# Optimization experiments

Measured on AMD Instinct MI355X. Metric: run time of the kernel, lower is better.

## Reference

```python
import jax, jax.numpy as jnp
import numpy as np

BOS = 1  # TOKENS['BOS'] assumed


def gru_scan(x_seq, h0, W_ih, W_hh, b_ih, b_hh):
    """PyTorch-style single-layer GRU over time. x_seq: (T,B,H), h0: (B,H)."""
    def step(h, x):
        gi = x @ W_ih.T + b_ih          # (B,3H)
        gh = h @ W_hh.T + b_hh          # (B,3H)
        i_r, i_z, i_n = jnp.split(gi, 3, axis=-1)
        h_r, h_z, h_n = jnp.split(gh, 3, axis=-1)
        r = jax.nn.sigmoid(i_r + h_r)
        z = jax.nn.sigmoid(i_z + h_z)
        n = jnp.tanh(i_n + r * h_n)
        h_new = (1.0 - z) * n + z * h
        return h_new, h_new
    hT, outs = jax.lax.scan(step, h0, x_seq)
    return outs, hT


def setup_inputs() -> dict:
    key = jax.random.key(0)
    ks = jax.random.split(key, 24)
    H = 256
    V = 50003       # user_size + 3
    TAGV = 966
    T_in, T_tgt, T_tag, B = 50, 40, 20, 32
    s = 0.02
    inp = {
        'input_tensor': jax.random.randint(ks[0], (T_in, B), 0, V),
        'target_tensor': jax.random.randint(ks[1], (T_tgt, B), 0, V),
        'tag_tensor': jax.random.randint(ks[2], (T_tag, B), 0, TAGV),
        'enc_emb': jax.random.normal(ks[3], (V, H), jnp.float32) * s,
        'enc_Wih': jax.random.normal(ks[4], (3 * H, H), jnp.float32) * s,
        'enc_Whh': jax.random.normal(ks[5], (3 * H, H), jnp.float32) * s,
        'enc_bih': jax.random.normal(ks[6], (3 * H,), jnp.float32) * s,
        'enc_bhh': jax.random.normal(ks[7], (3 * H,), jnp.float32) * s,
        'tag_emb': jax.random.normal(ks[8], (TAGV, H), jnp.float32) * s,
        'tag_Wih': jax.random.normal(ks[9], (3 * H, H), jnp.float32) * s,
        'tag_Whh': jax.random.normal(ks[10], (3 * H, H), jnp.float32) * s,
        'tag_bih': jax.random.normal(ks[11], (3 * H,), jnp.float32) * s,
        'tag_bhh': jax.random.normal(ks[12], (3 * H,), jnp.float32) * s,
        'proj_W': jax.random.normal(ks[13], (H, 2 * H), jnp.float32) * s,
        'proj_b': jax.random.normal(ks[14], (H,), jnp.float32) * s,
        'dec_Wih': jax.random.normal(ks[15], (3 * H, H), jnp.float32) * s,
        'dec_Whh': jax.random.normal(ks[16], (3 * H, H), jnp.float32) * s,
        'dec_bih': jax.random.normal(ks[17], (3 * H,), jnp.float32) * s,
        'dec_bhh': jax.random.normal(ks[18], (3 * H,), jnp.float32) * s,
        'out_W': jax.random.normal(ks[19], (V, H), jnp.float32) * s,
        'out_b': jax.random.normal(ks[20], (V,), jnp.float32) * s,
    }
    return inp


def reference(input_tensor, target_tensor, tag_tensor,
              enc_emb, enc_Wih, enc_Whh, enc_bih, enc_bhh,
              tag_emb, tag_Wih, tag_Whh, tag_bih, tag_bhh,
              proj_W, proj_b,
              dec_Wih, dec_Whh, dec_bih, dec_bhh,
              out_W, out_b):
    T_in, B = input_tensor.shape
    T_tgt = target_tensor.shape[0]
    H = enc_emb.shape[1]
    h0 = jnp.zeros((B, H), enc_emb.dtype)

    # encoder over input tokens
    _, enc_h = gru_scan(enc_emb[input_tensor], h0, enc_Wih, enc_Whh, enc_bih, enc_bhh)
    # tag encoder
    _, tag_h = gru_scan(tag_emb[tag_tensor], h0, tag_Wih, tag_Whh, tag_bih, tag_bhh)

    # proj(cat(tag_hidden, encoder_hidden)); dropout = identity (eval)
    merged = jnp.concatenate([tag_h, enc_h], axis=-1) @ proj_W.T + proj_b  # (B,H)

    # teacher forcing: decoder inputs = [BOS, target[:-1]]
    dec_in = jnp.concatenate(
        [jnp.full((1, B), BOS, dtype=target_tensor.dtype), target_tensor[:-1]], axis=0)
    dec_x = jax.nn.relu(enc_emb[dec_in])                 # (T_tgt,B,H), shared embedding
    dec_outs, _ = gru_scan(dec_x, merged, dec_Wih, dec_Whh, dec_bih, dec_bhh)
    logits = dec_outs @ out_W.T + out_b                  # (T_tgt,B,V)

    # criterion = CrossEntropyLoss(mean over batch), summed over timesteps
    logp = jax.nn.log_softmax(logits, axis=-1)
    nll = -jnp.take_along_axis(logp, target_tensor[..., None], axis=-1)[..., 0]  # (T_tgt,B)
    decoder_loss = nll.mean(axis=1).sum()
    avg_loss = decoder_loss / T_tgt
    decoder_outputs = logits[:, None, :, :]              # (T_tgt,1,B,V) like torch.stack of unsqueezed
    return (decoder_loss, avg_loss, decoder_outputs)
```

## Files before the change

### kernel.cpp

```cpp
#include <hip/hip_runtime.h>
#include <hip/hip_bf16.h>
#include <math.h>


#define H 256
#define H3 768
#define NBATCH 32
#define TIN 50
#define TTGT 40
#define TTAG 20
#define VSZ 50003
#define VP 50048
#define NT 782
#define MT 1280
#define NGI 330
#define NCVT 12512

typedef float f32x4 __attribute__((ext_vector_type(4)));
typedef short short8 __attribute__((ext_vector_type(8)));

__device__ __forceinline__ float dot4(float4 a, float4 b) {
    return a.x * b.x + a.y * b.y + a.z * b.z + a.w * b.w;
}

__device__ __forceinline__ void bar_lgkm() {
    asm volatile("s_waitcnt lgkmcnt(0)" ::: "memory");
    __builtin_amdgcn_s_barrier();
    __builtin_amdgcn_sched_barrier(0);
}

__global__ void k_prep(const float* eWih, const float* tWih, const float* dWih,
                       const float* projW, const float* eWhh, const float* tWhh,
                       const float* dWhh, float* d0, float* d1, float* d2,
                       float* d3, __hip_bfloat16* p0, __hip_bfloat16* p1,
                       __hip_bfloat16* p2) {
    int which = blockIdx.y;
    if (which < 4) {
        const float* s;
        float* d;
        int N, K;
        switch (which) {
            case 0: s = eWih; d = d0; N = H3; K = H; break;
            case 1: s = tWih; d = d1; N = H3; K = H; break;
            case 2: s = dWih; d = d2; N = H3; K = H; break;
            default: s = projW; d = d3; N = H; K = 2 * H; break;
        }
        int n = blockIdx.x;
        if (n >= N) return;
        for (int k = threadIdx.x; k < K; k += 256)
            d[(size_t)(k >> 2) * (N * 4) + n * 4 + (k & 3)] = s[(size_t)n * K + k];
    } else {
        if (blockIdx.x >= 96) return;
        const float* s = which == 4 ? eWhh : (which == 5 ? tWhh : dWhh);
        __hip_bfloat16* d = which == 4 ? p0 : (which == 5 ? p1 : p2);
        int idx = blockIdx.x * 256 + threadIdx.x;
        int lane = idx & 63;
        int f = (idx >> 6) % 48;
        int w = idx / (48 * 64);
        int ks = f / 6, rem = f % 6;
        int hf = rem / 3, q = rem % 3;
        int row = (q << 8) + (w << 5) + (hf << 4) + (lane & 15);
        int k = (ks << 5) + ((lane >> 4) << 3);
#pragma unroll
        for (int j = 0; j < 8; ++j)
            d[(size_t)idx * 8 + j] = __float2bfloat16(s[(size_t)row * H + k + j]);
    }
}

__global__ __launch_bounds__(256) void k_gi_cvt(
    const int* in_toks, const int* tag_toks, const int* tgt_toks,
    const float* enc_emb, const float* tag_emb, const float* W4e,
    const float* W4t, const float* W4d, const float* bih_e, const float* bhh_e,
    const float* bih_t, const float* bhh_t, const float* bih_d,
    const float* bhh_d, float* gi_e, float* gi_t, float* gi_d,
    const float* outW, __hip_bfloat16* outWb) {
    int bx = blockIdx.x, tid = threadIdx.x;
    if (bx >= NGI) {
        int i4 = ((bx - NGI) * 256 + tid) * 4;
        if (i4 >= VP * H) return;
        int row = i4 >> 8;
        float4 v;
        if (row < VSZ) v = *(const float4*)(outW + i4);
        else v = make_float4(0.f, 0.f, 0.f, 0.f);
        outWb[i4 + 0] = __float2bfloat16(v.x);
        outWb[i4 + 1] = __float2bfloat16(v.y);
        outWb[i4 + 2] = __float2bfloat16(v.z);
        outWb[i4 + 3] = __float2bfloat16(v.w);
        return;
    }
    __shared__ float x[NBATCH][H];
    int g = bx % 3, tt = bx / 3;
    const int* toks;
    const float* emb;
    const float* W4;
    const float* bihp;
    const float* bhhp;
    float* gip;
    int t, mode;
    if (tt < TIN) {
        toks = in_toks; emb = enc_emb; W4 = W4e; bihp = bih_e; bhhp = bhh_e;
        gip = gi_e; t = tt; mode = 0;
    } else if (tt < TIN + TTAG) {
        toks = tag_toks; emb = tag_emb; W4 = W4t; bihp = bih_t; bhhp = bhh_t;
        gip = gi_t; t = tt - TIN; mode = 0;
    } else {
        toks = tgt_toks; emb = enc_emb; W4 = W4d; bihp = bih_d; bhhp = bhh_d;
        gip = gi_d; t = tt - TIN - TTAG; mode = 2;
    }
    for (int b = 0; b < NBATCH; ++b) {
        int tok;
        if (mode == 2) tok = (t == 0) ? 1 : toks[(t - 1) * NBATCH + b];
        else tok = toks[t * NBATCH + b];
        float v = emb[(size_t)tok * H + tid];
        if (mode == 2) v = fmaxf(v, 0.0f);
        x[b][tid] = v;
    }
    __syncthreads();
    int nb_ = tid & 63, mg = tid >> 6;
    float acc[4][8];
#pragma unroll
    for (int j = 0; j < 4; ++j)
#pragma unroll
        for (int mi = 0; mi < 8; ++mi) acc[j][mi] = 0.f;
    for (int k4 = 0; k4 < 64; ++k4) {
        const float4* wrow = (const float4*)(W4 + (size_t)k4 * 3072);
        float4 w0 = wrow[g * 256 + nb_];
        float4 w1 = wrow[g * 256 + nb_ + 64];
        float4 w2 = wrow[g * 256 + nb_ + 128];
        float4 w3 = wrow[g * 256 + nb_ + 192];
#pragma unroll
        for (int mi = 0; mi < 8; ++mi) {
            float4 xv = *(const float4*)&x[mg * 8 + mi][k4 * 4];
            acc[0][mi] += dot4(xv, w0);
            acc[1][mi] += dot4(xv, w1);
            acc[2][mi] += dot4(xv, w2);
            acc[3][mi] += dot4(xv, w3);
        }
    }
#pragma unroll
    for (int j = 0; j < 4; ++j) {
        int n = g * 256 + nb_ + j * 64;
        float bv = bihp[n] + (g < 2 ? bhhp[n] : 0.0f);
        int nn = n & 255;
        int ww = nn >> 5, hf = (nn >> 4) & 1, lrr = nn & 15;
#pragma unroll
        for (int mi = 0; mi < 8; ++mi) {
            int bm = mg * 8 + mi;
            int locb = bm >> 4, lmm = bm & 15;
            int lgg = lmm >> 2, reg = lmm & 3;
            size_t idx = ((size_t)(t * 2 + locb) * 8 + ww) * 2048 +
                         hf * 1024 + reg * 256 + (lgg * 16 + lrr) * 4 + g;
            gip[idx] = acc[j][mi] + bv;
        }
    }
}

__global__ __launch_bounds__(512) void k_scan(
    int nset1,
    const float* gi1, const __hip_bfloat16* W1, const float* bhh1,
    const float* h01, float* hT1, __hip_bfloat16* out1, int T1,
    const float* gi2, const __hip_bfloat16* W2, const float* bhh2,
    const float* h02, float* hT2, __hip_bfloat16* out2, int T2) {
    __shared__ uint4 WL[8 * 12 * 64];
    __shared__ uint4 HBF[2][512];

    int blk = blockIdx.x, tid = threadIdx.x;
    const float *gip, *bhh, *h0;
    const __hip_bfloat16* Wg;
    float* hTp;
    __hip_bfloat16* outp;
    int T, loc;
    if (blk < nset1) {
        gip = gi1; Wg = W1; bhh = bhh1; h0 = h01; hTp = hT1; outp = out1;
        T = T1; loc = blk;
    } else {
        gip = gi2; Wg = W2; bhh = bhh2; h0 = h02; hTp = hT2; outp = out2;
        T = T2; loc = blk - nset1;
    }
    int mb = loc * 16;
    int w = tid >> 6, lane = tid & 63, lr = lane & 15, lg = lane >> 4;

    short8 wreg[36];
    const uint4* Wg4 = (const uint4*)Wg;
#pragma unroll
    for (int f = 0; f < 36; ++f) {
        uint4 v = Wg4[(size_t)(w * 48 + f) * 64 + lane];
        wreg[f] = *(short8*)&v;
    }
#pragma unroll
    for (int i = 0; i < 12; ++i)
        WL[(w * 12 + i) * 64 + lane] = Wg4[(size_t)(w * 48 + 36 + i) * 64 + lane];

    float bnv[2];
    bnv[0] = bhh[512 + w * 32 + lr];
    bnv[1] = bhh[512 + w * 32 + 16 + lr];

    float hprev[8];
    short* HB16 = (short*)HBF;
#pragma unroll
    for (int hf = 0; hf < 2; ++hf)
#pragma unroll
        for (int reg = 0; reg < 4; ++reg) {
            int row = lg * 4 + reg, col = w * 32 + hf * 16 + lr;
            float hv = h0 ? h0[(size_t)(mb + row) * H + col] : 0.0f;
            hprev[hf * 4 + reg] = hv;
            __hip_bfloat16 q = __float2bfloat16(hv);
            int slot = (w * 4 + hf * 2 + (lr >> 3)) ^ (row & 7);
            HB16[row * 256 + slot * 8 + (lr & 7)] = *(short*)&q;
        }
    float4 gv[8];
    {
        const float* gp = gip + ((size_t)loc * 8 + w) * 2048;
#pragma unroll
        for (int i = 0; i < 8; ++i)
            gv[i] = *(const float4*)(gp + (i >> 2) * 1024 + (i & 3) * 256 + lane * 4);
    }
    __syncthreads();

    const short8* HSbase = (const short8*)HBF;
    const short8* WLs = (const short8*)WL;
    for (int t = 0; t < T; ++t) {
        int p = t & 1, p2 = p ^ 1;
        const short8* HS = HSbase + p * 512;
        f32x4 acc[6];
        acc[0] = (f32x4){0.f, 0.f, 0.f, 0.f};
        acc[1] = acc[0];
        acc[2] = (f32x4){bnv[0], bnv[0], bnv[0], bnv[0]};
        acc[3] = acc[0];
        acc[4] = acc[0];
        acc[5] = (f32x4){bnv[1], bnv[1], bnv[1], bnv[1]};
#pragma unroll
        for (int ks = 0; ks < 6; ++ks) {
            short8 a = HS[lr * 32 + ((ks * 4 + lg) ^ (lr & 7))];
#pragma unroll
            for (int hf = 0; hf < 2; ++hf)
#pragma unroll
                for (int q = 0; q < 3; ++q)
                    acc[hf * 3 + q] = __builtin_amdgcn_mfma_f32_16x16x32_bf16(
                        a, wreg[ks * 6 + hf * 3 + q], acc[hf * 3 + q], 0, 0, 0);
        }
#pragma unroll
        for (int ks = 6; ks < 8; ++ks) {
            short8 a = HS[lr * 32 + ((ks * 4 + lg) ^ (lr & 7))];
#pragma unroll
            for (int hf = 0; hf < 2; ++hf)
#pragma unroll
                for (int q = 0; q < 3; ++q) {
                    short8 bv = WLs[(w * 12 + (ks - 6) * 6 + hf * 3 + q) * 64 + lane];
                    acc[hf * 3 + q] = __builtin_amdgcn_mfma_f32_16x16x32_bf16(
                        a, bv, acc[hf * 3 + q], 0, 0, 0);
                }
        }
#pragma unroll
        for (int hf = 0; hf < 2; ++hf)
#pragma unroll
            for (int reg = 0; reg < 4; ++reg) {
                float4 g4 = gv[hf * 4 + reg];
                float er = __expf(-(g4.x + acc[hf * 3 + 0][reg]));
                float r = __builtin_amdgcn_rcpf(1.0f + er);
                float ez = __expf(-(g4.y + acc[hf * 3 + 1][reg]));
                float z = __builtin_amdgcn_rcpf(1.0f + ez);
                float xx = g4.z + r * acc[hf * 3 + 2][reg];
                float e2 = __expf(-2.0f * fabsf(xx));
                float nv = copysignf((1.0f - e2) * __builtin_amdgcn_rcpf(1.0f + e2), xx);
                float hnew = (1.0f - z) * nv + z * hprev[hf * 4 + reg];
                hprev[hf * 4 + reg] = hnew;
                __hip_bfloat16 qb = __float2bfloat16(hnew);
                int row = lg * 4 + reg;
                int slot = (w * 4 + hf * 2 + (lr >> 3)) ^ (row & 7);
                HB16[p2 * 4096 + row * 256 + slot * 8 + (lr & 7)] = *(short*)&qb;
            }
        if (t + 1 < T) {
            const float* gp = gip + ((size_t)((t + 1) * 2 + loc) * 8 + w) * 2048;
#pragma unroll
            for (int i = 0; i < 8; ++i)
                gv[i] = *(const float4*)(gp + (i >> 2) * 1024 + (i & 3) * 256 + lane * 4);
        }
        if (outp && t >= 1) {
            int lb = tid >> 5, ch = tid & 31;
            short8 hv = HSbase[p * 512 + lb * 32 + (ch ^ (lb & 7))];
            *(short8*)(outp + (size_t)((t - 1) * NBATCH + mb + lb) * H + ch * 8) = hv;
        }
        bar_lgkm();
    }
    if (outp) {
        int lb = tid >> 5, ch = tid & 31;
        short8 hv = HSbase[(T & 1) * 512 + lb * 32 + (ch ^ (lb & 7))];
        *(short8*)(outp + (size_t)((T - 1) * NBATCH + mb + lb) * H + ch * 8) = hv;
    }
    if (hTp) {
#pragma unroll
        for (int hf = 0; hf < 2; ++hf)
#pragma unroll
            for (int reg = 0; reg < 4; ++reg) {
                int row = lg * 4 + reg, col = w * 32 + hf * 16 + lr;
                hTp[(size_t)(mb + row) * H + col] = hprev[hf * 4 + reg];
            }
    }
}

__global__ void k_proj(const float* tag_h, const float* enc_h,
                       const float* W4p, const float* pb, float* merged) {
    __shared__ float c[2 * H];
    int b = blockIdx.x, tid = threadIdx.x;
    c[tid] = tag_h[b * H + tid];
    c[H + tid] = enc_h[b * H + tid];
    __syncthreads();
    float acc = 0.f;
#pragma unroll 4
    for (int k4 = 0; k4 < 128; ++k4) {
        float4 cv = *(const float4*)&c[k4 * 4];
        float4 wv = ((const float4*)(W4p + (size_t)k4 * 1024))[tid];
        acc += dot4(cv, wv);
    }
    merged[b * H + tid] = acc + pb[tid];
}

__global__ __launch_bounds__(256) void k_logits(const __hip_bfloat16* A,
                                                const __hip_bfloat16* Bw,
                                                const float* bias, float* dout,
                                                float* pmax, float* psum) {
    __shared__ uint4 bsm[2048];
    __shared__ float cst[4][16][68];
    int bid = blockIdx.x;
    int wg = (bid & 7) * 1955 + (bid >> 3);
    int nblk = wg / 20, mblk = wg % 20;
    int m0 = mblk * 64, n0 = nblk * 64;
    int tid = threadIdx.x;
    int wave = tid >> 6, lane = tid & 63, lr = lane & 15, lg = lane >> 4;
    const uint4* Bg = (const uint4*)(Bw + (size_t)n0 * H);
#pragma unroll
    for (int i = 0; i < 8; ++i) {
        int c = tid + i * 256;
        int r = c >> 5, g = c & 31;
        bsm[(r << 5) | (g ^ (r & 7))] = Bg[c];
    }
    short8 areg[8];
    const uint4* Ar = (const uint4*)(A + (size_t)(m0 + wave * 16 + lr) * H);
#pragma unroll
    for (int ks = 0; ks < 8; ++ks) {
        uint4 v = Ar[ks * 4 + lg];
        areg[ks] = *(short8*)&v;
    }
    float biasv[4];
    bool valid[4];
#pragma unroll
    for (int ns = 0; ns < 4; ++ns) {
        int n = n0 + ns * 16 + lr;
        valid[ns] = (n < VSZ);
        biasv[ns] = valid[ns] ? bias[n] : 0.f;
    }
    __syncthreads();
    f32x4 acc[4];
#pragma unroll
    for (int ns = 0; ns < 4; ++ns) acc[ns] = (f32x4){0.f, 0.f, 0.f, 0.f};
    const short8* L = (const short8*)bsm;
#pragma unroll
    for (int ks = 0; ks < 8; ++ks) {
        int ga = ks * 4 + lg;
#pragma unroll
        for (int ns = 0; ns < 4; ++ns) {
            int rb = ns * 16 + lr;
            acc[ns] = __builtin_amdgcn_mfma_f32_16x16x32_bf16(
                areg[ks], L[(rb << 5) | (ga ^ (rb & 7))], acc[ns], 0, 0, 0);
        }
    }
    float* cw = &cst[wave][0][0];
#pragma unroll
    for (int reg = 0; reg < 4; ++reg) {
        int m = m0 + wave * 16 + lg * 4 + reg;
        float v[4];
        float rm = -INFINITY;
#pragma unroll
        for (int ns = 0; ns < 4; ++ns) {
            v[ns] = acc[ns][reg] + biasv[ns];
            if (valid[ns]) rm = fmaxf(rm, v[ns]);
            cw[(lg * 4 + reg) * 68 + ns * 16 + lr] = v[ns];
        }
        for (int off = 1; off < 16; off <<= 1) rm = fmaxf(rm, __shfl_xor(rm, off));
        float se = 0.f;
#pragma unroll
        for (int ns = 0; ns < 4; ++ns)
            if (valid[ns]) se += __expf(v[ns] - rm);
        for (int off = 1; off < 16; off <<= 1) se += __shfl_xor(se, off);
        if (lr == 0) {
            pmax[(size_t)m * NT + nblk] = rm;
            psum[(size_t)m * NT + nblk] = se;
        }
    }
    float* dbase = dout + 2 + (size_t)(m0 + wave * 16) * VSZ + n0;
    bool colok = (n0 + lane < VSZ);
#pragma unroll
    for (int rl = 0; rl < 16; ++rl) {
        float val = cst[wave][rl][lane];
        if (colok) dbase[(size_t)rl * VSZ + lane] = val;
    }
}

__global__ void k_lse(const float* pmax, const float* psum, float* lse) {
    int m = blockIdx.x, tid = threadIdx.x;
    __shared__ float sm[4];
    float lm = -INFINITY;
    for (int i = tid; i < NT; i += 256) lm = fmaxf(lm, pmax[(size_t)m * NT + i]);
    for (int off = 1; off < 64; off <<= 1) lm = fmaxf(lm, __shfl_xor(lm, off));
    if ((tid & 63) == 0) sm[tid >> 6] = lm;
    __syncthreads();
    float M = fmaxf(fmaxf(sm[0], sm[1]), fmaxf(sm[2], sm[3]));
    __syncthreads();
    float s = 0.f;
    for (int i = tid; i < NT; i += 256)
        s += psum[(size_t)m * NT + i] * __expf(pmax[(size_t)m * NT + i] - M);
    for (int off = 1; off < 64; off <<= 1) s += __shfl_xor(s, off);
    if ((tid & 63) == 0) sm[tid >> 6] = s;
    __syncthreads();
    if (tid == 0) lse[m] = M + logf(sm[0] + sm[1] + sm[2] + sm[3]);
}

__global__ void k_loss(const float* lse, const int* tgt, float* dout) {
    int tid = threadIdx.x;
    __shared__ float sm[4];
    float s = 0.f;
    for (int m = tid; m < MT; m += 256) {
        int tg = tgt[m];
        s += lse[m] - dout[2 + (size_t)m * VSZ + tg];
    }
    for (int off = 1; off < 64; off <<= 1) s += __shfl_xor(s, off);
    if ((tid & 63) == 0) sm[tid >> 6] = s;
    __syncthreads();
    if (tid == 0) {
        float total = sm[0] + sm[1] + sm[2] + sm[3];
        dout[0] = total / 32.0f;
        dout[1] = total / 1280.0f;
    }
}

extern "C" void kernel_launch(void* const* d_in, const int* in_sizes, int n_in,
                              void* d_out, int out_size, void* d_ws,
                              size_t ws_size, hipStream_t stream) {
    const int* input_tensor = (const int*)d_in[0];
    const int* target_tensor = (const int*)d_in[1];
    const int* tag_tensor = (const int*)d_in[2];
    const float* enc_emb = (const float*)d_in[3];
    const float* enc_Wih = (const float*)d_in[4];
    const float* enc_Whh = (const float*)d_in[5];
    const float* enc_bih = (const float*)d_in[6];
    const float* enc_bhh = (const float*)d_in[7];
    const float* tag_emb = (const float*)d_in[8];
    const float* tag_Wih = (const float*)d_in[9];
    const float* tag_Whh = (const float*)d_in[10];
    const float* tag_bih = (const float*)d_in[11];
    const float* tag_bhh = (const float*)d_in[12];
    const float* proj_W = (const float*)d_in[13];
    const float* proj_b = (const float*)d_in[14];
    const float* dec_Wih = (const float*)d_in[15];
    const float* dec_Whh = (const float*)d_in[16];
    const float* dec_bih = (const float*)d_in[17];
    const float* dec_bhh = (const float*)d_in[18];
    const float* out_W = (const float*)d_in[19];
    const float* out_b = (const float*)d_in[20];

    char* wsb = (char*)d_ws;
    size_t o = 0;
    auto alloc = [&](size_t bytes) {
        size_t r = o;
        o += (bytes + 511) & ~(size_t)511;
        return r;
    };
    float* W4_enc_ih = (float*)(wsb + alloc(H3 * H * 4));
    float* W4_tag_ih = (float*)(wsb + alloc(H3 * H * 4));
    float* W4_dec_ih = (float*)(wsb + alloc(H3 * H * 4));
    float* W4_proj   = (float*)(wsb + alloc(H * 2 * H * 4));
    float* gi_enc = (float*)(wsb + alloc((size_t)TIN * 131072));
    float* gi_tag = (float*)(wsb + alloc((size_t)TTAG * 131072));
    float* gi_dec = (float*)(wsb + alloc((size_t)TTGT * 131072));
    float* enc_h  = (float*)(wsb + alloc(NBATCH * H * 4));
    float* tag_h  = (float*)(wsb + alloc(NBATCH * H * 4));
    float* merged = (float*)(wsb + alloc(NBATCH * H * 4));
    float* lse    = (float*)(wsb + alloc(MT * 4));
    __hip_bfloat16* Wp_enc = (__hip_bfloat16*)(wsb + alloc(H3 * H * 2));
    __hip_bfloat16* Wp_tag = (__hip_bfloat16*)(wsb + alloc(H3 * H * 2));
    __hip_bfloat16* Wp_dec = (__hip_bfloat16*)(wsb + alloc(H3 * H * 2));
    __hip_bfloat16* outWb  = (__hip_bfloat16*)(wsb + alloc((size_t)VP * H * 2));
    __hip_bfloat16* decA   = (__hip_bfloat16*)(wsb + alloc((size_t)MT * H * 2));
    float* pmax = (float*)(wsb + alloc((size_t)MT * NT * 4));
    float* psum = (float*)(wsb + alloc((size_t)MT * NT * 4));

    float* dout = (float*)d_out;

    k_prep<<<dim3(H3, 7), 256, 0, stream>>>(
        enc_Wih, tag_Wih, dec_Wih, proj_W, enc_Whh, tag_Whh, dec_Whh,
        W4_enc_ih, W4_tag_ih, W4_dec_ih, W4_proj, Wp_enc, Wp_tag, Wp_dec);

    k_gi_cvt<<<NGI + NCVT, 256, 0, stream>>>(
        input_tensor, tag_tensor, target_tensor, enc_emb, tag_emb, W4_enc_ih,
        W4_tag_ih, W4_dec_ih, enc_bih, enc_bhh, tag_bih, tag_bhh, dec_bih,
        dec_bhh, gi_enc, gi_tag, gi_dec, out_W, outWb);

    k_scan<<<4, 512, 0, stream>>>(
        2, gi_enc, Wp_enc, enc_bhh, nullptr, enc_h, nullptr, TIN,
        gi_tag, Wp_tag, tag_bhh, nullptr, tag_h, nullptr, TTAG);

    k_proj<<<NBATCH, 256, 0, stream>>>(tag_h, enc_h, W4_proj, proj_b, merged);

    k_scan<<<2, 512, 0, stream>>>(
        2, gi_dec, Wp_dec, dec_bhh, merged, nullptr, decA, TTGT,
        nullptr, nullptr, nullptr, nullptr, nullptr, nullptr, 0);

    k_logits<<<NT * 20, 256, 0, stream>>>(decA, outWb, out_b, dout, pmax, psum);

    k_lse<<<MT, 256, 0, stream>>>(pmax, psum, lse);

    k_loss<<<1, 256, 0, stream>>>(lse, target_tensor, dout);
}
```

Measured before the change: 506.5 us.

## Fuse decoder scan with logits GEMM via progress flags and bf16 gate inputs

Merges the decoder GRU scan and the vocabulary logits GEMM into one kernel. Two scan blocks publish per-timestep progress through atomic flags, and the GEMM blocks spin-wait on those flags, so the logit tiles for early timesteps can start while later timesteps are still being computed. The precomputed input-gate activations are stored in bf16 instead of fp32 to cut scan-side memory traffic. More recurrent weight fragments are kept in registers rather than LDS, and the logits tiles are widened to 512 threads covering two M blocks. This risks deadlock if the scan blocks are not scheduled ahead of the spinning GEMM blocks, and adds bf16 rounding to the gate inputs.

```diff
diff --git a/kernel.cpp b/kernel.cpp
--- a/kernel.cpp
+++ b/kernel.cpp
@@ -23,6 +23,11 @@
     return a.x * b.x + a.y * b.y + a.z * b.z + a.w * b.w;
 }
 
+__device__ __forceinline__ float bf2f(short s) {
+    unsigned int u = ((unsigned int)(unsigned short)s) << 16;
+    return __builtin_bit_cast(float, u);
+}
+
 __device__ __forceinline__ void bar_lgkm() {
     asm volatile("s_waitcnt lgkmcnt(0)" ::: "memory");
     __builtin_amdgcn_s_barrier();
@@ -33,8 +38,10 @@
                        const float* projW, const float* eWhh, const float* tWhh,
                        const float* dWhh, float* d0, float* d1, float* d2,
                        float* d3, __hip_bfloat16* p0, __hip_bfloat16* p1,
-                       __hip_bfloat16* p2) {
+                       __hip_bfloat16* p2, int* prog) {
     int which = blockIdx.y;
+    if (which == 0 && blockIdx.x == 0 && threadIdx.x < 2)
+        prog[threadIdx.x] = 0;
     if (which < 4) {
         const float* s;
         float* d;
@@ -72,8 +79,8 @@
     const float* enc_emb, const float* tag_emb, const float* W4e,
     const float* W4t, const float* W4d, const float* bih_e, const float* bhh_e,
     const float* bih_t, const float* bhh_t, const float* bih_d,
-    const float* bhh_d, float* gi_e, float* gi_t, float* gi_d,
-    const float* outW, __hip_bfloat16* outWb) {
+    const float* bhh_d, __hip_bfloat16* gi_e, __hip_bfloat16* gi_t,
+    __hip_bfloat16* gi_d, const float* outW, __hip_bfloat16* outWb) {
     int bx = blockIdx.x, tid = threadIdx.x;
     if (bx >= NGI) {
         int i4 = ((bx - NGI) * 256 + tid) * 4;
@@ -95,7 +102,7 @@
     const float* W4;
     const float* bihp;
     const float* bhhp;
-    float* gip;
+    __hip_bfloat16* gip;
     int t, mode;
     if (tt < TIN) {
         toks = in_toks; emb = enc_emb; W4 = W4e; bihp = bih_e; bhhp = bhh_e;
@@ -150,46 +157,43 @@
             int lgg = lmm >> 2, reg = lmm & 3;
             size_t idx = ((size_t)(t * 2 + locb) * 8 + ww) * 2048 +
                          hf * 1024 + reg * 256 + (lgg * 16 + lrr) * 4 + g;
-            gip[idx] = acc[j][mi] + bv;
+            gip[idx] = __float2bfloat16(acc[j][mi] + bv);
         }
     }
 }
 
 __global__ __launch_bounds__(512) void k_scan(
     int nset1,
-    const float* gi1, const __hip_bfloat16* W1, const float* bhh1,
-    const float* h01, float* hT1, __hip_bfloat16* out1, int T1,
-    const float* gi2, const __hip_bfloat16* W2, const float* bhh2,
-    const float* h02, float* hT2, __hip_bfloat16* out2, int T2) {
-    __shared__ uint4 WL[8 * 12 * 64];
+    const __hip_bfloat16* gi1, const __hip_bfloat16* W1, const float* bhh1,
+    float* hT1, int T1,
+    const __hip_bfloat16* gi2, const __hip_bfloat16* W2, const float* bhh2,
+    float* hT2, int T2) {
+    __shared__ uint4 WL[6 * 8 * 64];
     __shared__ uint4 HBF[2][512];
 
     int blk = blockIdx.x, tid = threadIdx.x;
-    const float *gip, *bhh, *h0;
-    const __hip_bfloat16* Wg;
+    const __hip_bfloat16 *gip, *Wg;
+    const float* bhh;
     float* hTp;
-    __hip_bfloat16* outp;
     int T, loc;
     if (blk < nset1) {
-        gip = gi1; Wg = W1; bhh = bhh1; h0 = h01; hTp = hT1; outp = out1;
-        T = T1; loc = blk;
+        gip = gi1; Wg = W1; bhh = bhh1; hTp = hT1; T = T1; loc = blk;
     } else {
-        gip = gi2; Wg = W2; bhh = bhh2; h0 = h02; hTp = hT2; outp = out2;
-        T = T2; loc = blk - nset1;
+        gip = gi2; Wg = W2; bhh = bhh2; hTp = hT2; T = T2; loc = blk - nset1;
     }
     int mb = loc * 16;
     int w = tid >> 6, lane = tid & 63, lr = lane & 15, lg = lane >> 4;
 
-    short8 wreg[36];
+    short8 wreg[42];
     const uint4* Wg4 = (const uint4*)Wg;
 #pragma unroll
-    for (int f = 0; f < 36; ++f) {
+    for (int f = 0; f < 42; ++f) {
         uint4 v = Wg4[(size_t)(w * 48 + f) * 64 + lane];
         wreg[f] = *(short8*)&v;
     }
 #pragma unroll
-    for (int i = 0; i < 12; ++i)
-        WL[(w * 12 + i) * 64 + lane] = Wg4[(size_t)(w * 48 + 36 + i) * 64 + lane];
+    for (int i = 0; i < 6; ++i)
+        WL[(w * 6 + i) * 64 + lane] = Wg4[(size_t)(w * 48 + 42 + i) * 64 + lane];
 
     float bnv[2];
     bnv[0] = bhh[512 + w * 32 + lr];
@@ -201,19 +205,17 @@
     for (int hf = 0; hf < 2; ++hf)
 #pragma unroll
         for (int reg = 0; reg < 4; ++reg) {
-            int row = lg * 4 + reg, col = w * 32 + hf * 16 + lr;
-            float hv = h0 ? h0[(size_t)(mb + row) * H + col] : 0.0f;
-            hprev[hf * 4 + reg] = hv;
-            __hip_bfloat16 q = __float2bfloat16(hv);
+            int row = lg * 4 + reg;
+            hprev[hf * 4 + reg] = 0.0f;
             int slot = (w * 4 + hf * 2 + (lr >> 3)) ^ (row & 7);
-            HB16[row * 256 + slot * 8 + (lr & 7)] = *(short*)&q;
-        }
-    float4 gv[8];
+            HB16[row * 256 + slot * 8 + (lr & 7)] = 0;
+        }
+    uint2 gv[8];
     {
-        const float* gp = gip + ((size_t)loc * 8 + w) * 2048;
+        const __hip_bfloat16* gp = gip + ((size_t)loc * 8 + w) * 2048;
 #pragma unroll
         for (int i = 0; i < 8; ++i)
-            gv[i] = *(const float4*)(gp + (i >> 2) * 1024 + (i & 3) * 256 + lane * 4);
+            gv[i] = *(const uint2*)(gp + (i >> 2) * 1024 + (i & 3) * 256 + lane * 4);
     }
     __syncthreads();
 
@@ -230,7 +232,7 @@
         acc[4] = acc[0];
         acc[5] = (f32x4){bnv[1], bnv[1], bnv[1], bnv[1]};
 #pragma unroll
-        for (int ks = 0; ks < 6; ++ks) {
+        for (int ks = 0; ks < 7; ++ks) {
             short8 a = HS[lr * 32 + ((ks * 4 + lg) ^ (lr & 7))];
 #pragma unroll
             for (int hf = 0; hf < 2; ++hf)
@@ -239,14 +241,13 @@
                     acc[hf * 3 + q] = __builtin_amdgcn_mfma_f32_16x16x32_bf16(
                         a, wreg[ks * 6 + hf * 3 + q], acc[hf * 3 + q], 0, 0, 0);
         }
-#pragma unroll
-        for (int ks = 6; ks < 8; ++ks) {
-            short8 a = HS[lr * 32 + ((ks * 4 + lg) ^ (lr & 7))];
+        {
+            short8 a = HS[lr * 32 + ((28 + lg) ^ (lr & 7))];
 #pragma unroll
             for (int hf = 0; hf < 2; ++hf)
 #pragma unroll
                 for (int q = 0; q < 3; ++q) {
-                    short8 bv = WLs[(w * 12 + (ks - 6) * 6 + hf * 3 + q) * 64 + lane];
+                    short8 bv = WLs[(w * 6 + hf * 3 + q) * 64 + lane];
                     acc[hf * 3 + q] = __builtin_amdgcn_mfma_f32_16x16x32_bf16(
                         a, bv, acc[hf * 3 + q], 0, 0, 0);
                 }
@@ -255,12 +256,15 @@
         for (int hf = 0; hf < 2; ++hf)
 #pragma unroll
             for (int reg = 0; reg < 4; ++reg) {
-                float4 g4 = gv[hf * 4 + reg];
-                float er = __expf(-(g4.x + acc[hf * 3 + 0][reg]));
+                uint2 u = gv[hf * 4 + reg];
+                float gr = bf2f((short)(u.x & 0xffff));
+                float gz = bf2f((short)(u.x >> 16));
+                float gn = bf2f((short)(u.y & 0xffff));
+                float er = __expf(-(gr + acc[hf * 3 + 0][reg]));
                 float r = __builtin_amdgcn_rcpf(1.0f + er);
-                float ez = __expf(-(g4.y + acc[hf * 3 + 1][reg]));
+                float ez = __expf(-(gz + acc[hf * 3 + 1][reg]));
                 float z = __builtin_amdgcn_rcpf(1.0f + ez);
-                float xx = g4.z + r * acc[hf * 3 + 2][reg];
+                float xx = gn + r * acc[hf * 3 + 2][reg];
                 float e2 = __expf(-2.0f * fabsf(xx));
                 float nv = copysignf((1.0f - e2) * __builtin_amdgcn_rcpf(1.0f + e2), xx);
                 float hnew = (1.0f - z) * nv + z * hprev[hf * 4 + reg];
@@ -271,22 +275,13 @@
                 HB16[p2 * 4096 + row * 256 + slot * 8 + (lr & 7)] = *(short*)&qb;
             }
         if (t + 1 < T) {
-            const float* gp = gip + ((size_t)((t + 1) * 2 + loc) * 8 + w) * 2048;
+            const __hip_bfloat16* gp =
+                gip + ((size_t)((t + 1) * 2 + loc) * 8 + w) * 2048;
 #pragma unroll
             for (int i = 0; i < 8; ++i)
-                gv[i] = *(const float4*)(gp + (i >> 2) * 1024 + (i & 3) * 256 + lane * 4);
-        }
-        if (outp && t >= 1) {
-            int lb = tid >> 5, ch = tid & 31;
-            short8 hv = HSbase[p * 512 + lb * 32 + (ch ^ (lb & 7))];
-            *(short8*)(outp + (size_t)((t - 1) * NBATCH + mb + lb) * H + ch * 8) = hv;
+                gv[i] = *(const uint2*)(gp + (i >> 2) * 1024 + (i & 3) * 256 + lane * 4);
         }
         bar_lgkm();
-    }
-    if (outp) {
-        int lb = tid >> 5, ch = tid & 31;
-        short8 hv = HSbase[(T & 1) * 512 + lb * 32 + (ch ^ (lb & 7))];
-        *(short8*)(outp + (size_t)((T - 1) * NBATCH + mb + lb) * H + ch * 8) = hv;
     }
     if (hTp) {
 #pragma unroll
@@ -316,31 +311,165 @@
     merged[b * H + tid] = acc + pb[tid];
 }
 
-__global__ __launch_bounds__(256) void k_logits(const __hip_bfloat16* A,
-                                                const __hip_bfloat16* Bw,
-                                                const float* bias, float* dout,
-                                                float* pmax, float* psum) {
-    __shared__ uint4 bsm[2048];
-    __shared__ float cst[4][16][68];
-    int bid = blockIdx.x;
-    int wg = (bid & 7) * 1955 + (bid >> 3);
-    int nblk = wg / 20, mblk = wg % 20;
-    int m0 = mblk * 64, n0 = nblk * 64;
+__global__ __launch_bounds__(512) void k_declog(
+    const __hip_bfloat16* gi_dec, const __hip_bfloat16* Wdec,
+    const float* dec_bhh, const float* merged, __hip_bfloat16* decA,
+    int* prog, const __hip_bfloat16* Bw, const float* bias, float* dout,
+    float* pmax, float* psum) {
+    __shared__ __align__(16) char smem[67584];
     int tid = threadIdx.x;
     int wave = tid >> 6, lane = tid & 63, lr = lane & 15, lg = lane >> 4;
+
+    if (blockIdx.x < 2) {
+        uint4* WL = (uint4*)smem;
+        uint4* HBF = (uint4*)(smem + 49152);
+        short* HB16 = (short*)HBF;
+        int loc = blockIdx.x, mb = loc * 16, w = wave;
+        const int T = TTGT;
+
+        short8 wreg[42];
+        const uint4* Wg4 = (const uint4*)Wdec;
+#pragma unroll
+        for (int f = 0; f < 42; ++f) {
+            uint4 v = Wg4[(size_t)(w * 48 + f) * 64 + lane];
+            wreg[f] = *(short8*)&v;
+        }
+#pragma unroll
+        for (int i = 0; i < 6; ++i)
+            WL[(w * 6 + i) * 64 + lane] =
+                Wg4[(size_t)(w * 48 + 42 + i) * 64 + lane];
+
+        float bnv[2];
+        bnv[0] = dec_bhh[512 + w * 32 + lr];
+        bnv[1] = dec_bhh[512 + w * 32 + 16 + lr];
+
+        float hprev[8];
+#pragma unroll
+        for (int hf = 0; hf < 2; ++hf)
+#pragma unroll
+            for (int reg = 0; reg < 4; ++reg) {
+                int row = lg * 4 + reg, col = w * 32 + hf * 16 + lr;
+                float hv = merged[(size_t)(mb + row) * H + col];
+                hprev[hf * 4 + reg] = hv;
+                __hip_bfloat16 q = __float2bfloat16(hv);
+                int slot = (w * 4 + hf * 2 + (lr >> 3)) ^ (row & 7);
+                HB16[row * 256 + slot * 8 + (lr & 7)] = *(short*)&q;
+            }
+        uint2 gv[8];
+        {
+            const __hip_bfloat16* gp = gi_dec + ((size_t)loc * 8 + w) * 2048;
+#pragma unroll
+            for (int i = 0; i < 8; ++i)
+                gv[i] = *(const uint2*)(gp + (i >> 2) * 1024 + (i & 3) * 256 + lane * 4);
+        }
+        __syncthreads();
+
+        const short8* HSbase = (const short8*)HBF;
+        const short8* WLs = (const short8*)WL;
+        for (int t = 0; t < T; ++t) {
+            int p = t & 1, p2 = p ^ 1;
+            const short8* HS = HSbase + p * 512;
+            f32x4 acc[6];
+            acc[0] = (f32x4){0.f, 0.f, 0.f, 0.f};
+            acc[1] = acc[0];
+            acc[2] = (f32x4){bnv[0], bnv[0], bnv[0], bnv[0]};
+            acc[3] = acc[0];
+            acc[4] = acc[0];
+            acc[5] = (f32x4){bnv[1], bnv[1], bnv[1], bnv[1]};
+#pragma unroll
+            for (int ks = 0; ks < 7; ++ks) {
+                short8 a = HS[lr * 32 + ((ks * 4 + lg) ^ (lr & 7))];
+#pragma unroll
+                for (int hf = 0; hf < 2; ++hf)
+#pragma unroll
+                    for (int q = 0; q < 3; ++q)
+                        acc[hf * 3 + q] = __builtin_amdgcn_mfma_f32_16x16x32_bf16(
+                            a, wreg[ks * 6 + hf * 3 + q], acc[hf * 3 + q], 0, 0, 0);
+            }
+            {
+                short8 a = HS[lr * 32 + ((28 + lg) ^ (lr & 7))];
+#pragma unroll
+                for (int hf = 0; hf < 2; ++hf)
+#pragma unroll
+                    for (int q = 0; q < 3; ++q) {
+                        short8 bv = WLs[(w * 6 + hf * 3 + q) * 64 + lane];
+                        acc[hf * 3 + q] = __builtin_amdgcn_mfma_f32_16x16x32_bf16(
+                            a, bv, acc[hf * 3 + q], 0, 0, 0);
+                    }
+            }
+#pragma unroll
+            for (int hf = 0; hf < 2; ++hf)
+#pragma unroll
+                for (int reg = 0; reg < 4; ++reg) {
+                    uint2 u = gv[hf * 4 + reg];
+                    float gr = bf2f((short)(u.x & 0xffff));
+                    float gz = bf2f((short)(u.x >> 16));
+                    float gn = bf2f((short)(u.y & 0xffff));
+                    float er = __expf(-(gr + acc[hf * 3 + 0][reg]));
+                    float r = __builtin_amdgcn_rcpf(1.0f + er);
+                    float ez = __expf(-(gz + acc[hf * 3 + 1][reg]));
+                    float z = __builtin_amdgcn_rcpf(1.0f + ez);
+                    float xx = gn + r * acc[hf * 3 + 2][reg];
+                    float e2 = __expf(-2.0f * fabsf(xx));
+                    float nv = copysignf(
+                        (1.0f - e2) * __builtin_amdgcn_rcpf(1.0f + e2), xx);
+                    float hnew = (1.0f - z) * nv + z * hprev[hf * 4 + reg];
+                    hprev[hf * 4 + reg] = hnew;
+                    __hip_bfloat16 qb = __float2bfloat16(hnew);
+                    int row = lg * 4 + reg;
+                    int slot = (w * 4 + hf * 2 + (lr >> 3)) ^ (row & 7);
+                    HB16[p2 * 4096 + row * 256 + slot * 8 + (lr & 7)] = *(short*)&qb;
+                }
+            if (t >= 1) {
+                int lb = tid >> 5, ch = tid & 31;
+                short8 hv = HSbase[p * 512 + lb * 32 + (ch ^ (lb & 7))];
+                *(short8*)(decA + (size_t)((t - 1) * NBATCH + mb + lb) * H + ch * 8) = hv;
+            }
+            bool pub = ((t & 1) == 0) && t >= 2;
+            if (pub) asm volatile("s_waitcnt vmcnt(0)" ::: "memory");
+            if (t + 1 < T) {
+                const __hip_bfloat16* gp =
+                    gi_dec + ((size_t)((t + 1) * 2 + loc) * 8 + w) * 2048;
+#pragma unroll
+                for (int i = 0; i < 8; ++i)
+                    gv[i] = *(const uint2*)(gp + (i >> 2) * 1024 + (i & 3) * 256 + lane * 4);
+            }
+            bar_lgkm();
+            if (pub && tid == 0) {
+                __threadfence();
+                __hip_atomic_store(&prog[loc], t, __ATOMIC_RELEASE,
+                                   __HIP_MEMORY_SCOPE_AGENT);
+            }
+        }
+        {
+            int lb = tid >> 5, ch = tid & 31;
+            short8 hv = HSbase[(T & 1) * 512 + lb * 32 + (ch ^ (lb & 7))];
+            *(short8*)(decA + (size_t)((T - 1) * NBATCH + mb + lb) * H + ch * 8) = hv;
+        }
+        asm volatile("s_waitcnt vmcnt(0)" ::: "memory");
+        __syncthreads();
+        if (tid == 0) {
+            __threadfence();
+            __hip_atomic_store(&prog[loc], TTGT, __ATOMIC_RELEASE,
+                               __HIP_MEMORY_SCOPE_AGENT);
+        }
+        return;
+    }
+
+    uint4* bsm = (uint4*)smem;
+    float* cst = (float*)(smem + 32768);
+    int lbid = blockIdx.x - 2;
+    int mpair = lbid / NT, nblk = lbid % NT;
+    int wg2 = wave >> 2, wsub = wave & 3;
+    int mblk = mpair * 2 + wg2;
+    int m0 = mblk * 64, n0 = nblk * 64;
+
     const uint4* Bg = (const uint4*)(Bw + (size_t)n0 * H);
 #pragma unroll
-    for (int i = 0; i < 8; ++i) {
-        int c = tid + i * 256;
+    for (int i = 0; i < 4; ++i) {
+        int c = tid + i * 512;
         int r = c >> 5, g = c & 31;
         bsm[(r << 5) | (g ^ (r & 7))] = Bg[c];
-    }
-    short8 areg[8];
-    const uint4* Ar = (const uint4*)(A + (size_t)(m0 + wave * 16 + lr) * H);
-#pragma unroll
-    for (int ks = 0; ks < 8; ++ks) {
-        uint4 v = Ar[ks * 4 + lg];
-        areg[ks] = *(short8*)&v;
     }
     float biasv[4];
     bool valid[4];
@@ -350,7 +479,23 @@
         valid[ns] = (n < VSZ);
         biasv[ns] = valid[ns] ? bias[n] : 0.f;
     }
-    __syncthreads();
+    if (tid == 0) {
+        int need = 4 * mpair + 4;
+        while (__hip_atomic_load(&prog[0], __ATOMIC_ACQUIRE,
+                                 __HIP_MEMORY_SCOPE_AGENT) < need ||
+               __hip_atomic_load(&prog[1], __ATOMIC_ACQUIRE,
+                                 __HIP_MEMORY_SCOPE_AGENT) < need)
+            __builtin_amdgcn_s_sleep(8);
+    }
+    __syncthreads();
+
+    short8 areg[8];
+    const uint4* Ar = (const uint4*)(decA + (size_t)(m0 + wsub * 16 + lr) * H);
+#pragma unroll
+    for (int ks = 0; ks < 8; ++ks) {
+        uint4 v = Ar[ks * 4 + lg];
+        areg[ks] = *(short8*)&v;
+    }
     f32x4 acc[4];
 #pragma unroll
     for (int ns = 0; ns < 4; ++ns) acc[ns] = (f32x4){0.f, 0.f, 0.f, 0.f};
@@ -365,10 +510,10 @@
                 areg[ks], L[(rb << 5) | (ga ^ (rb & 7))], acc[ns], 0, 0, 0);
         }
     }
-    float* cw = &cst[wave][0][0];
+    float* cw = cst + wave * (16 * 68);
 #pragma unroll
     for (int reg = 0; reg < 4; ++reg) {
-        int m = m0 + wave * 16 + lg * 4 + reg;
+        int m = m0 + wsub * 16 + lg * 4 + reg;
         float v[4];
         float rm = -INFINITY;
 #pragma unroll
@@ -388,11 +533,11 @@
             psum[(size_t)m * NT + nblk] = se;
         }
     }
-    float* dbase = dout + 2 + (size_t)(m0 + wave * 16) * VSZ + n0;
+    float* dbase = dout + 2 + (size_t)(m0 + wsub * 16) * VSZ + n0;
     bool colok = (n0 + lane < VSZ);
 #pragma unroll
     for (int rl = 0; rl < 16; ++rl) {
-        float val = cst[wave][rl][lane];
+        float val = cw[rl * 68 + lane];
         if (colok) dbase[(size_t)rl * VSZ + lane] = val;
     }
 }
@@ -470,13 +615,14 @@
     float* W4_tag_ih = (float*)(wsb + alloc(H3 * H * 4));
     float* W4_dec_ih = (float*)(wsb + alloc(H3 * H * 4));
     float* W4_proj   = (float*)(wsb + alloc(H * 2 * H * 4));
-    float* gi_enc = (float*)(wsb + alloc((size_t)TIN * 131072));
-    float* gi_tag = (float*)(wsb + alloc((size_t)TTAG * 131072));
-    float* gi_dec = (float*)(wsb + alloc((size_t)TTGT * 131072));
+    __hip_bfloat16* gi_enc = (__hip_bfloat16*)(wsb + alloc((size_t)TIN * 65536));
+    __hip_bfloat16* gi_tag = (__hip_bfloat16*)(wsb + alloc((size_t)TTAG * 65536));
+    __hip_bfloat16* gi_dec = (__hip_bfloat16*)(wsb + alloc((size_t)TTGT * 65536));
     float* enc_h  = (float*)(wsb + alloc(NBATCH * H * 4));
     float* tag_h  = (float*)(wsb + alloc(NBATCH * H * 4));
     float* merged = (float*)(wsb + alloc(NBATCH * H * 4));
     float* lse    = (float*)(wsb + alloc(MT * 4));
+    int*   prog   = (int*)(wsb + alloc(64 * 4));
     __hip_bfloat16* Wp_enc = (__hip_bfloat16*)(wsb + alloc(H3 * H * 2));
     __hip_bfloat16* Wp_tag = (__hip_bfloat16*)(wsb + alloc(H3 * H * 2));
     __hip_bfloat16* Wp_dec = (__hip_bfloat16*)(wsb + alloc(H3 * H * 2));
@@ -489,7 +635,8 @@
 
     k_prep<<<dim3(H3, 7), 256, 0, stream>>>(
         enc_Wih, tag_Wih, dec_Wih, proj_W, enc_Whh, tag_Whh, dec_Whh,
-        W4_enc_ih, W4_tag_ih, W4_dec_ih, W4_proj, Wp_enc, Wp_tag, Wp_dec);
+        W4_enc_ih, W4_tag_ih, W4_dec_ih, W4_proj, Wp_enc, Wp_tag, Wp_dec,
+        prog);
 
     k_gi_cvt<<<NGI + NCVT, 256, 0, stream>>>(
         input_tensor, tag_tensor, target_tensor, enc_emb, tag_emb, W4_enc_ih,
@@ -497,16 +644,14 @@
         dec_bhh, gi_enc, gi_tag, gi_dec, out_W, outWb);
 
     k_scan<<<4, 512, 0, stream>>>(
-        2, gi_enc, Wp_enc, enc_bhh, nullptr, enc_h, nullptr, TIN,
-        gi_tag, Wp_tag, tag_bhh, nullptr, tag_h, nullptr, TTAG);
+        2, gi_enc, Wp_enc, enc_bhh, enc_h, TIN,
+        gi_tag, Wp_tag, tag_bhh, tag_h, TTAG);
 
     k_proj<<<NBATCH, 256, 0, stream>>>(tag_h, enc_h, W4_proj, proj_b, merged);
 
-    k_scan<<<2, 512, 0, stream>>>(
-        2, gi_dec, Wp_dec, dec_bhh, merged, nullptr, decA, TTGT,
-        nullptr, nullptr, nullptr, nullptr, nullptr, nullptr, 0);
-
-    k_logits<<<NT * 20, 256, 0, stream>>>(decA, outWb, out_b, dout, pmax, psum);
+    k_declog<<<2 + 10 * NT, 512, 0, stream>>>(
+        gi_dec, Wp_dec, dec_bhh, merged, decA, prog, outWb, out_b, dout,
+        pmax, psum);
 
     k_lse<<<MT, 256, 0, stream>>>(pmax, psum, lse);
 
```

After: 608.4 us. 20.1% more time.

## Split GRU scan across 16 waves with bf16 gate inputs and streaming logits stores

Applied to the files above, without the earlier changes.

The recurrent scan kernel now uses 1024 threads (16 waves), each owning 16 hidden columns instead of 32. This halves the per-wave MFMA chain and register-held weights on the latency-bound serial recurrence. The precomputed input-gate activations are stored and read as bf16 instead of fp32, halving their traffic, at some cost in precision. Logit stores use nontemporal hints to avoid polluting cache with the large output.

```diff
diff --git a/kernel.cpp b/kernel.cpp
--- a/kernel.cpp
+++ b/kernel.cpp
@@ -21,6 +21,11 @@
 
 __device__ __forceinline__ float dot4(float4 a, float4 b) {
     return a.x * b.x + a.y * b.y + a.z * b.z + a.w * b.w;
+}
+
+__device__ __forceinline__ float bf2f(short s) {
+    unsigned int u = ((unsigned int)(unsigned short)s) << 16;
+    return __builtin_bit_cast(float, u);
 }
 
 __device__ __forceinline__ void bar_lgkm() {
@@ -55,11 +60,10 @@
         __hip_bfloat16* d = which == 4 ? p0 : (which == 5 ? p1 : p2);
         int idx = blockIdx.x * 256 + threadIdx.x;
         int lane = idx & 63;
-        int f = (idx >> 6) % 48;
-        int w = idx / (48 * 64);
-        int ks = f / 6, rem = f % 6;
-        int hf = rem / 3, q = rem % 3;
-        int row = (q << 8) + (w << 5) + (hf << 4) + (lane & 15);
+        int f = (idx >> 6) % 24;
+        int w = idx / (24 * 64);
+        int ks = f / 3, q = f % 3;
+        int row = (q << 8) + (w << 4) + (lane & 15);
         int k = (ks << 5) + ((lane >> 4) << 3);
 #pragma unroll
         for (int j = 0; j < 8; ++j)
@@ -72,8 +76,8 @@
     const float* enc_emb, const float* tag_emb, const float* W4e,
     const float* W4t, const float* W4d, const float* bih_e, const float* bhh_e,
     const float* bih_t, const float* bhh_t, const float* bih_d,
-    const float* bhh_d, float* gi_e, float* gi_t, float* gi_d,
-    const float* outW, __hip_bfloat16* outWb) {
+    const float* bhh_d, __hip_bfloat16* gi_e, __hip_bfloat16* gi_t,
+    __hip_bfloat16* gi_d, const float* outW, __hip_bfloat16* outWb) {
     int bx = blockIdx.x, tid = threadIdx.x;
     if (bx >= NGI) {
         int i4 = ((bx - NGI) * 256 + tid) * 4;
@@ -95,7 +99,7 @@
     const float* W4;
     const float* bihp;
     const float* bhhp;
-    float* gip;
+    __hip_bfloat16* gip;
     int t, mode;
     if (tt < TIN) {
         toks = in_toks; emb = enc_emb; W4 = W4e; bihp = bih_e; bhhp = bhh_e;
@@ -142,31 +146,31 @@
         int n = g * 256 + nb_ + j * 64;
         float bv = bihp[n] + (g < 2 ? bhhp[n] : 0.0f);
         int nn = n & 255;
-        int ww = nn >> 5, hf = (nn >> 4) & 1, lrr = nn & 15;
+        int ww = nn >> 4, lrr = nn & 15;
 #pragma unroll
         for (int mi = 0; mi < 8; ++mi) {
             int bm = mg * 8 + mi;
             int locb = bm >> 4, lmm = bm & 15;
             int lgg = lmm >> 2, reg = lmm & 3;
-            size_t idx = ((size_t)(t * 2 + locb) * 8 + ww) * 2048 +
-                         hf * 1024 + reg * 256 + (lgg * 16 + lrr) * 4 + g;
-            gip[idx] = acc[j][mi] + bv;
-        }
-    }
-}
-
-__global__ __launch_bounds__(512) void k_scan(
+            size_t idx = ((size_t)(t * 2 + locb) * 16 + ww) * 1024 +
+                         reg * 256 + (lgg * 16 + lrr) * 4 + g;
+            gip[idx] = __float2bfloat16(acc[j][mi] + bv);
+        }
+    }
+}
+
+__global__ __launch_bounds__(1024) void k_scan(
     int nset1,
-    const float* gi1, const __hip_bfloat16* W1, const float* bhh1,
+    const __hip_bfloat16* gi1, const __hip_bfloat16* W1, const float* bhh1,
     const float* h01, float* hT1, __hip_bfloat16* out1, int T1,
-    const float* gi2, const __hip_bfloat16* W2, const float* bhh2,
+    const __hip_bfloat16* gi2, const __hip_bfloat16* W2, const float* bhh2,
     const float* h02, float* hT2, __hip_bfloat16* out2, int T2) {
-    __shared__ uint4 WL[8 * 12 * 64];
+    __shared__ uint4 WL[16 * 6 * 64];
     __shared__ uint4 HBF[2][512];
 
     int blk = blockIdx.x, tid = threadIdx.x;
-    const float *gip, *bhh, *h0;
-    const __hip_bfloat16* Wg;
+    const __hip_bfloat16 *gip, *Wg;
+    const float *bhh, *h0;
     float* hTp;
     __hip_bfloat16* outp;
     int T, loc;
@@ -180,40 +184,37 @@
     int mb = loc * 16;
     int w = tid >> 6, lane = tid & 63, lr = lane & 15, lg = lane >> 4;
 
-    short8 wreg[36];
+    short8 wreg[18];
     const uint4* Wg4 = (const uint4*)Wg;
 #pragma unroll
-    for (int f = 0; f < 36; ++f) {
-        uint4 v = Wg4[(size_t)(w * 48 + f) * 64 + lane];
+    for (int f = 0; f < 18; ++f) {
+        uint4 v = Wg4[(size_t)(w * 24 + f) * 64 + lane];
         wreg[f] = *(short8*)&v;
     }
 #pragma unroll
-    for (int i = 0; i < 12; ++i)
-        WL[(w * 12 + i) * 64 + lane] = Wg4[(size_t)(w * 48 + 36 + i) * 64 + lane];
-
-    float bnv[2];
-    bnv[0] = bhh[512 + w * 32 + lr];
-    bnv[1] = bhh[512 + w * 32 + 16 + lr];
-
-    float hprev[8];
+    for (int i = 0; i < 6; ++i)
+        WL[(w * 6 + i) * 64 + lane] = Wg4[(size_t)(w * 24 + 18 + i) * 64 + lane];
+
+    float bnv = bhh[512 + w * 16 + lr];
+
+    float hprev[4];
     short* HB16 = (short*)HBF;
 #pragma unroll
-    for (int hf = 0; hf < 2; ++hf)
-#pragma unroll
-        for (int reg = 0; reg < 4; ++reg) {
-            int row = lg * 4 + reg, col = w * 32 + hf * 16 + lr;
-            float hv = h0 ? h0[(size_t)(mb + row) * H + col] : 0.0f;
-            hprev[hf * 4 + reg] = hv;
-            __hip_bfloat16 q = __float2bfloat16(hv);
-            int slot = (w * 4 + hf * 2 + (lr >> 3)) ^ (row & 7);
-            HB16[row * 256 + slot * 8 + (lr & 7)] = *(short*)&q;
-        }
-    float4 gv[8];
+    for (int reg = 0; reg < 4; ++reg) {
+        int row = lg * 4 + reg, col = w * 16 + lr;
+        float hv = h0 ? h0[(size_t)(mb + row) * H + col] : 0.0f;
+        hprev[reg] = hv;
+        __hip_bfloat16 q = __float2bfloat16(hv);
+        int ch = w * 2 + (lr >> 3);
+        int slot = ch ^ (row & 7);
+        HB16[row * 256 + slot * 8 + (lr & 7)] = *(short*)&q;
+    }
+    uint2 gv[4];
     {
-        const float* gp = gip + ((size_t)loc * 8 + w) * 2048;
-#pragma unroll
-        for (int i = 0; i < 8; ++i)
-            gv[i] = *(const float4*)(gp + (i >> 2) * 1024 + (i & 3) * 256 + lane * 4);
+        const __hip_bfloat16* gp = gip + ((size_t)loc * 16 + w) * 1024;
+#pragma unroll
+        for (int reg = 0; reg < 4; ++reg)
+            gv[reg] = *(const uint2*)(gp + reg * 256 + lane * 4);
     }
     __syncthreads();
 
@@ -222,80 +223,74 @@
     for (int t = 0; t < T; ++t) {
         int p = t & 1, p2 = p ^ 1;
         const short8* HS = HSbase + p * 512;
-        f32x4 acc[6];
+        f32x4 acc[3];
         acc[0] = (f32x4){0.f, 0.f, 0.f, 0.f};
         acc[1] = acc[0];
-        acc[2] = (f32x4){bnv[0], bnv[0], bnv[0], bnv[0]};
-        acc[3] = acc[0];
-        acc[4] = acc[0];
-        acc[5] = (f32x4){bnv[1], bnv[1], bnv[1], bnv[1]};
+        acc[2] = (f32x4){bnv, bnv, bnv, bnv};
 #pragma unroll
         for (int ks = 0; ks < 6; ++ks) {
             short8 a = HS[lr * 32 + ((ks * 4 + lg) ^ (lr & 7))];
 #pragma unroll
-            for (int hf = 0; hf < 2; ++hf)
-#pragma unroll
-                for (int q = 0; q < 3; ++q)
-                    acc[hf * 3 + q] = __builtin_amdgcn_mfma_f32_16x16x32_bf16(
-                        a, wreg[ks * 6 + hf * 3 + q], acc[hf * 3 + q], 0, 0, 0);
+            for (int q = 0; q < 3; ++q)
+                acc[q] = __builtin_amdgcn_mfma_f32_16x16x32_bf16(
+                    a, wreg[ks * 3 + q], acc[q], 0, 0, 0);
         }
 #pragma unroll
         for (int ks = 6; ks < 8; ++ks) {
             short8 a = HS[lr * 32 + ((ks * 4 + lg) ^ (lr & 7))];
 #pragma unroll
-            for (int hf = 0; hf < 2; ++hf)
-#pragma unroll
-                for (int q = 0; q < 3; ++q) {
-                    short8 bv = WLs[(w * 12 + (ks - 6) * 6 + hf * 3 + q) * 64 + lane];
-                    acc[hf * 3 + q] = __builtin_amdgcn_mfma_f32_16x16x32_bf16(
-                        a, bv, acc[hf * 3 + q], 0, 0, 0);
-                }
-        }
-#pragma unroll
-        for (int hf = 0; hf < 2; ++hf)
-#pragma unroll
-            for (int reg = 0; reg < 4; ++reg) {
-                float4 g4 = gv[hf * 4 + reg];
-                float er = __expf(-(g4.x + acc[hf * 3 + 0][reg]));
-                float r = __builtin_amdgcn_rcpf(1.0f + er);
-                float ez = __expf(-(g4.y + acc[hf * 3 + 1][reg]));
-                float z = __builtin_amdgcn_rcpf(1.0f + ez);
-                float xx = g4.z + r * acc[hf * 3 + 2][reg];
-                float e2 = __expf(-2.0f * fabsf(xx));
-                float nv = copysignf((1.0f - e2) * __builtin_amdgcn_rcpf(1.0f + e2), xx);
-                float hnew = (1.0f - z) * nv + z * hprev[hf * 4 + reg];
-                hprev[hf * 4 + reg] = hnew;
-                __hip_bfloat16 qb = __float2bfloat16(hnew);
-                int row = lg * 4 + reg;
-                int slot = (w * 4 + hf * 2 + (lr >> 3)) ^ (row & 7);
-                HB16[p2 * 4096 + row * 256 + slot * 8 + (lr & 7)] = *(short*)&qb;
+            for (int q = 0; q < 3; ++q) {
+                short8 bv = WLs[(w * 6 + (ks - 6) * 3 + q) * 64 + lane];
+                acc[q] = __builtin_amdgcn_mfma_f32_16x16x32_bf16(
+                    a, bv, acc[q], 0, 0, 0);
             }
+        }
+#pragma unroll
+        for (int reg = 0; reg < 4; ++reg) {
+            uint2 u = gv[reg];
+            float gr = bf2f((short)(u.x & 0xffff));
+            float gz = bf2f((short)(u.x >> 16));
+            float gn = bf2f((short)(u.y & 0xffff));
+            float er = __expf(-(gr + acc[0][reg]));
+            float r = __builtin_amdgcn_rcpf(1.0f + er);
+            float ez = __expf(-(gz + acc[1][reg]));
+            float z = __builtin_amdgcn_rcpf(1.0f + ez);
+            float xx = gn + r * acc[2][reg];
+            float e2 = __expf(-2.0f * fabsf(xx));
+            float nv = copysignf((1.0f - e2) * __builtin_amdgcn_rcpf(1.0f + e2), xx);
+            float hnew = (1.0f - z) * nv + z * hprev[reg];
+            hprev[reg] = hnew;
+            __hip_bfloat16 qb = __float2bfloat16(hnew);
+            int row = lg * 4 + reg;
+            int ch = w * 2 + (lr >> 3);
+            int slot = ch ^ (row & 7);
+            HB16[p2 * 4096 + row * 256 + slot * 8 + (lr & 7)] = *(short*)&qb;
+        }
         if (t + 1 < T) {
-            const float* gp = gip + ((size_t)((t + 1) * 2 + loc) * 8 + w) * 2048;
-#pragma unroll
-            for (int i = 0; i < 8; ++i)
-                gv[i] = *(const float4*)(gp + (i >> 2) * 1024 + (i & 3) * 256 + lane * 4);
-        }
-        if (outp && t >= 1) {
-            int lb = tid >> 5, ch = tid & 31;
-            short8 hv = HSbase[p * 512 + lb * 32 + (ch ^ (lb & 7))];
-            *(short8*)(outp + (size_t)((t - 1) * NBATCH + mb + lb) * H + ch * 8) = hv;
+            const __hip_bfloat16* gp =
+                gip + ((size_t)((t + 1) * 2 + loc) * 16 + w) * 1024;
+#pragma unroll
+            for (int reg = 0; reg < 4; ++reg)
+                gv[reg] = *(const uint2*)(gp + reg * 256 + lane * 4);
+        }
+        if (outp && t >= 1 && tid < 512) {
+            int lb = tid >> 5, ch2 = tid & 31;
+            short8 hv = HSbase[p * 512 + lb * 32 + (ch2 ^ (lb & 7))];
+            *(short8*)(outp + (size_t)((t - 1) * NBATCH + mb + lb) * H + ch2 * 8) = hv;
         }
         bar_lgkm();
     }
-    if (outp) {
-        int lb = tid >> 5, ch = tid & 31;
-        short8 hv = HSbase[(T & 1) * 512 + lb * 32 + (ch ^ (lb & 7))];
-        *(short8*)(outp + (size_t)((T - 1) * NBATCH + mb + lb) * H + ch * 8) = hv;
+    if (outp && tid < 512) {
+        int lb = tid >> 5, ch2 = tid & 31;
+        short8 hv = HSbase[(T & 1) * 512 + lb * 32 + (ch2 ^ (lb & 7))];
+        *(short8*)(outp + (size_t)((T - 1) * NBATCH + mb + lb) * H + ch2 * 8) = hv;
     }
     if (hTp) {
 #pragma unroll
-        for (int hf = 0; hf < 2; ++hf)
-#pragma unroll
-            for (int reg = 0; reg < 4; ++reg) {
-                int row = lg * 4 + reg, col = w * 32 + hf * 16 + lr;
-                hTp[(size_t)(mb + row) * H + col] = hprev[hf * 4 + reg];
-            }
+        for (int reg = 0; reg < 4; ++reg) {
+            int row = lg * 4 + reg, col = w * 16 + lr;
+            hTp[(size_t)(mb + row) * H + col] = hprev[reg];
+        }
     }
 }
 
@@ -393,7 +388,8 @@
 #pragma unroll
     for (int rl = 0; rl < 16; ++rl) {
         float val = cst[wave][rl][lane];
-        if (colok) dbase[(size_t)rl * VSZ + lane] = val;
+        if (colok)
+            __builtin_nontemporal_store(val, &dbase[(size_t)rl * VSZ + lane]);
     }
 }
 
@@ -470,9 +466,9 @@
     float* W4_tag_ih = (float*)(wsb + alloc(H3 * H * 4));
     float* W4_dec_ih = (float*)(wsb + alloc(H3 * H * 4));
     float* W4_proj   = (float*)(wsb + alloc(H * 2 * H * 4));
-    float* gi_enc = (float*)(wsb + alloc((size_t)TIN * 131072));
-    float* gi_tag = (float*)(wsb + alloc((size_t)TTAG * 131072));
-    float* gi_dec = (float*)(wsb + alloc((size_t)TTGT * 131072));
+    __hip_bfloat16* gi_enc = (__hip_bfloat16*)(wsb + alloc((size_t)TIN * 65536));
+    __hip_bfloat16* gi_tag = (__hip_bfloat16*)(wsb + alloc((size_t)TTAG * 65536));
+    __hip_bfloat16* gi_dec = (__hip_bfloat16*)(wsb + alloc((size_t)TTGT * 65536));
     float* enc_h  = (float*)(wsb + alloc(NBATCH * H * 4));
     float* tag_h  = (float*)(wsb + alloc(NBATCH * H * 4));
     float* merged = (float*)(wsb + alloc(NBATCH * H * 4));
@@ -496,13 +492,13 @@
         W4_tag_ih, W4_dec_ih, enc_bih, enc_bhh, tag_bih, tag_bhh, dec_bih,
         dec_bhh, gi_enc, gi_tag, gi_dec, out_W, outWb);
 
-    k_scan<<<4, 512, 0, stream>>>(
+    k_scan<<<4, 1024, 0, stream>>>(
         2, gi_enc, Wp_enc, enc_bhh, nullptr, enc_h, nullptr, TIN,
         gi_tag, Wp_tag, tag_bhh, nullptr, tag_h, nullptr, TTAG);
 
     k_proj<<<NBATCH, 256, 0, stream>>>(tag_h, enc_h, W4_proj, proj_b, merged);
 
-    k_scan<<<2, 512, 0, stream>>>(
+    k_scan<<<2, 1024, 0, stream>>>(
         2, gi_dec, Wp_dec, dec_bhh, merged, nullptr, decA, TTGT,
         nullptr, nullptr, nullptr, nullptr, nullptr, nullptr, 0);
 
```

Result: faster. 448.0 us (-11.6%).
